# Kernel tuning notes

Hardware: AMD Instinct MI355X
Metric: run time of the kernel (lower is better)

## Reference

```python
import jax, jax.numpy as jnp
import numpy as np

N_PATCH, N_Z, K, BS = 16, 128, 10, 1024
D = N_PATCH * N_Z


def setup_inputs() -> dict:
    key = jax.random.key(0)
    k1, k2, k3, k4 = jax.random.split(key, 4)
    z = jax.random.normal(k1, (BS, D), dtype=jnp.float32)
    m = jax.random.normal(k2, (K, D), dtype=jnp.float32)
    L = jax.random.normal(k3, (K, D, D), dtype=jnp.float32)
    components = jax.random.randint(k4, (BS,), 0, K, dtype=jnp.int64)
    return {"z": z, "m": m, "L": L, "components": components}


def reference(z, m, L, components):
    # samps[k] = m[k] + z @ L[k].T   -> (K, BS, D)
    samps = jnp.einsum('bd,ked->kbe', z, L) + m[:, None, :]
    # one-hot mask-and-sum over components == gather selected expert per sample
    x = samps[components, jnp.arange(z.shape[0])]  # (BS, D)
    return x.reshape(-1, N_PATCH, N_Z)
```

## Files before the change

kernel.cpp:

```cpp
#include <hip/hip_runtime.h>
#include <hip/hip_bf16.h>


#define DDIM  2048
#define BSAMP 1024
#define KCOMP 10
#define MPAD  160

typedef __attribute__((ext_vector_type(8))) short bf16x8;
typedef __attribute__((ext_vector_type(4))) float f32x4;

__device__ __forceinline__ short bfs(float x) {
    __hip_bfloat16 h = __float2bfloat16(x);
    return *reinterpret_cast<short*>(&h);
}

__global__ void build_map(const int* __restrict__ comp,
                          int* __restrict__ rowmap,
                          int* __restrict__ counts) {
    __shared__ int sc[KCOMP];
    const int t = threadIdx.x;
    if (t < KCOMP) sc[t] = 0;
    __syncthreads();
    const int c = comp[t];
    const int r = atomicAdd(&sc[c], 1);
    if (r < MPAD) rowmap[c * MPAD + r] = t;
    __syncthreads();
    if (t < KCOMP) counts[t] = sc[t];
}

__global__ void zprep(const float* __restrict__ z,
                      const int* __restrict__ rowmap,
                      short* __restrict__ zfrag) {
    const int idx  = blockIdx.x * 256 + threadIdx.x;
    const int lane = idx & 63;
    const int rest = idx >> 6;
    const int ms   = rest % 10;
    const int kit  = rest / 10;
    const int it   = kit & 63;
    const int k    = kit >> 6;
    const int slot = ms * 16 + (lane & 15);
    const int r    = rowmap[k * MPAD + slot] & (BSAMP - 1);
    const int d    = it * 32 + (lane >> 4) * 8;
    const float* zp = z + (size_t)r * DDIM + d;
    f32x4 a = *(const f32x4*)zp;
    f32x4 b = *(const f32x4*)(zp + 4);
    bf16x8 o;
#pragma unroll
    for (int j = 0; j < 4; ++j) { o[j] = bfs(a[j]); o[4 + j] = bfs(b[j]); }
    *(bf16x8*)(zfrag + (size_t)idx * 8) = o;
}

template <int MT>
__device__ __forceinline__ void gmm_body(
        const short* __restrict__ Ap,
        const float* __restrict__ Bp,
        const float* __restrict__ mvec,
        const int* __restrict__ rowmap,
        float* __restrict__ out,
        int k, int mh, int e, int cnt, int lane) {
    f32x4 acc[MT];
#pragma unroll
    for (int mt = 0; mt < MT; ++mt) acc[mt] = (f32x4){0.f, 0.f, 0.f, 0.f};

    f32x4 Bw[8][2];
    bf16x8 A0[MT], A1[MT];
#pragma unroll
    for (int j = 0; j < 8; ++j) {
        Bw[j][0] = *(const f32x4*)(Bp + j * 32);
        Bw[j][1] = *(const f32x4*)(Bp + j * 32 + 4);
    }
#pragma unroll
    for (int mt = 0; mt < MT; ++mt) A0[mt] = *(const bf16x8*)(Ap + mt * 512);

    const float* Bpf = Bp + 8 * 32;
    const short* Apf = Ap + 5120;
    int it = 0;

    auto step = [&](bf16x8* Ac, bf16x8* An, f32x4* Bs) {
#pragma unroll
        for (int mt = 0; mt < MT; ++mt) An[mt] = *(const bf16x8*)(Apf + mt * 512);
        f32x4 nb0 = *(const f32x4*)(Bpf);
        f32x4 nb1 = *(const f32x4*)(Bpf + 4);
        bf16x8 b;
#pragma unroll
        for (int j = 0; j < 4; ++j) { b[j] = bfs(Bs[0][j]); b[4 + j] = bfs(Bs[1][j]); }
#pragma unroll
        for (int mt = 0; mt < MT; ++mt)
            acc[mt] = __builtin_amdgcn_mfma_f32_16x16x32_bf16(Ac[mt], b, acc[mt], 0, 0, 0);
        Bs[0] = nb0; Bs[1] = nb1;
        ++it;
        if (it < 63) Apf += 5120;
        if (it < 56) Bpf += 32;
    };

    for (int ot = 0; ot < 8; ++ot) {
        step(A0, A1, Bw[0]); step(A1, A0, Bw[1]);
        step(A0, A1, Bw[2]); step(A1, A0, Bw[3]);
        step(A0, A1, Bw[4]); step(A1, A0, Bw[5]);
        step(A0, A1, Bw[6]); step(A1, A0, Bw[7]);
    }

    const float mu  = mvec[k * DDIM + e];
    const int rquad = (lane >> 4) * 4;
    const int rmB   = k * MPAD;
#pragma unroll
    for (int mt = 0; mt < MT; ++mt) {
        const int sb = mh * 80 + mt * 16 + rquad;
#pragma unroll
        for (int r = 0; r < 4; ++r) {
            const int slot = sb + r;
            if (slot < cnt) {
                const int bidx = rowmap[rmB + slot];
                out[(size_t)bidx * DDIM + e] = acc[mt][r] + mu;
            }
        }
    }
}

__global__ __launch_bounds__(128, 2)
void gmm_direct(const short* __restrict__ zfrag,
                const float* __restrict__ mvec,
                const float* __restrict__ Lmat,
                const int* __restrict__ rowmap,
                const int* __restrict__ counts,
                float* __restrict__ out) {
    const int t = threadIdx.x, lane = t & 63, nh = t >> 6;
    const int n  = blockIdx.x >> 1;
    const int mh = blockIdx.x & 1;
    const int k  = blockIdx.y;
    const int cnt = counts[k];
    const int rem = cnt - mh * 80;
    if (rem <= 0) return;
    const int nmt = (rem >= 80) ? 5 : ((rem + 15) >> 4);

    const int e = n * 32 + nh * 16 + (lane & 15);
    const short* Ap = zfrag + ((size_t)(k * 64) * 10 + mh * 5) * 512 + lane * 8;
    const float* Bp = Lmat + (size_t)k * DDIM * DDIM + (size_t)e * DDIM
                    + (lane >> 4) * 8;

    switch (nmt) {
        case 5: gmm_body<5>(Ap, Bp, mvec, rowmap, out, k, mh, e, cnt, lane); break;
        case 4: gmm_body<4>(Ap, Bp, mvec, rowmap, out, k, mh, e, cnt, lane); break;
        case 3: gmm_body<3>(Ap, Bp, mvec, rowmap, out, k, mh, e, cnt, lane); break;
        case 2: gmm_body<2>(Ap, Bp, mvec, rowmap, out, k, mh, e, cnt, lane); break;
        default: gmm_body<1>(Ap, Bp, mvec, rowmap, out, k, mh, e, cnt, lane); break;
    }
}

__device__ __forceinline__ void async16(void* lds, const void* g) {
    __builtin_amdgcn_global_load_lds(
        (const __attribute__((address_space(1))) void*)g,
        (__attribute__((address_space(3))) void*)lds, 16, 0, 0);
}
__device__ __forceinline__ bf16x8 frag8(const char* base, int o0, int o1) {
    f32x4 x = *(const f32x4*)(base + o0);
    f32x4 y = *(const f32x4*)(base + o1);
    bf16x8 r;
#pragma unroll
    for (int i = 0; i < 4; ++i) { r[i] = bfs(x[i]); r[4 + i] = bfs(y[i]); }
    return r;
}
__global__ __launch_bounds__(256, 2)
void gmm_f32z(const float* __restrict__ z, const float* __restrict__ mvec,
              const float* __restrict__ Lmat, const int* __restrict__ rowmap,
              const int* __restrict__ counts, float* __restrict__ out) {
    __shared__ __attribute__((aligned(16))) char smem[2 * 28672];
    const int t = threadIdx.x, lane = t & 63, w = t >> 6;
    const int mh = w >> 1, nh = w & 1;
    const int k = blockIdx.y, n0 = blockIdx.x * 64;
    const float* Lk = Lmat + (size_t)k * DDIM * DDIM;
    const int rq = t >> 3;
    const int scol = ((t & 7) ^ (rq & 7)) * 4;
    int rm[5];
#pragma unroll
    for (int j = 0; j < 5; ++j)
        rm[j] = rowmap[k * MPAD + j * 32 + rq] & (BSAMP - 1);
    const unsigned ub = (unsigned)(t & ~63) * 16;
    auto stage = [&](int buf, int it) {
        char* lb = smem + buf * 28672;
        const int d0 = it * 32 + scol;
#pragma unroll
        for (int j = 0; j < 5; ++j)
            async16(lb + j * 4096 + ub, z + (size_t)rm[j] * DDIM + d0);
        async16(lb + 20480 + ub,        Lk + (size_t)(n0 + rq) * DDIM + d0);
        async16(lb + 20480 + 4096 + ub, Lk + (size_t)(n0 + 32 + rq) * DDIM + d0);
    };
    f32x4 acc[5][2];
#pragma unroll
    for (int mt = 0; mt < 5; ++mt)
#pragma unroll
        for (int nt = 0; nt < 2; ++nt) acc[mt][nt] = (f32x4){0.f, 0.f, 0.f, 0.f};
    stage(0, 0);
    __syncthreads();
    const int fr = lane & 15, g0 = (lane >> 4) * 2;
    for (int it = 0; it < DDIM / 32; ++it) {
        if (it + 1 < DDIM / 32) stage((it + 1) & 1, it + 1);
        const char* lb = smem + (it & 1) * 28672;
        const int rb0 = nh * 32 + fr, rb1 = rb0 + 16;
        bf16x8 b0 = frag8(lb + 20480, rb0 * 128 + ((g0 ^ rb0) & 7) * 16,
                          rb0 * 128 + (((g0 + 1) ^ rb0) & 7) * 16);
        bf16x8 b1 = frag8(lb + 20480, rb1 * 128 + ((g0 ^ rb1) & 7) * 16,
                          rb1 * 128 + (((g0 + 1) ^ rb1) & 7) * 16);
#pragma unroll
        for (int mt = 0; mt < 5; ++mt) {
            const int ra = mh * 80 + mt * 16 + fr;
            bf16x8 a = frag8(lb, ra * 128 + ((g0 ^ ra) & 7) * 16,
                             ra * 128 + (((g0 + 1) ^ ra) & 7) * 16);
            acc[mt][0] = __builtin_amdgcn_mfma_f32_16x16x32_bf16(a, b0, acc[mt][0], 0, 0, 0);
            acc[mt][1] = __builtin_amdgcn_mfma_f32_16x16x32_bf16(a, b1, acc[mt][1], 0, 0, 0);
        }
        __syncthreads();
    }
    const int cnt = counts[k], rquad = (lane >> 4) * 4;
#pragma unroll
    for (int nt = 0; nt < 2; ++nt) {
        const int e = n0 + nh * 32 + nt * 16 + fr;
        const float mu = mvec[k * DDIM + e];
#pragma unroll
        for (int mt = 0; mt < 5; ++mt) {
            const int sb = mh * 80 + mt * 16 + rquad;
#pragma unroll
            for (int r = 0; r < 4; ++r) {
                const int slot = sb + r;
                if (slot < cnt)
                    out[(size_t)rowmap[k * MPAD + slot] * DDIM + e] = acc[mt][nt][r] + mu;
            }
        }
    }
}

extern "C" void kernel_launch(void* const* d_in, const int* in_sizes, int n_in,
                              void* d_out, int out_size, void* d_ws, size_t ws_size,
                              hipStream_t stream) {
    const float* z    = (const float*)d_in[0];
    const float* mvec = (const float*)d_in[1];
    const float* Lmat = (const float*)d_in[2];
    const int* comp   = (const int*)d_in[3];
    float* out        = (float*)d_out;

    int* rowmap = (int*)d_ws;
    int* counts = rowmap + KCOMP * MPAD;
    build_map<<<1, BSAMP, 0, stream>>>(comp, rowmap, counts);

    const size_t zf_off = 8192;
    const size_t zf_sz  = (size_t)KCOMP * 64 * 10 * 64 * 16;

    if (ws_size >= zf_off + zf_sz) {
        short* zfrag = (short*)((char*)d_ws + zf_off);
        zprep<<<1600, 256, 0, stream>>>(z, rowmap, zfrag);
        gmm_direct<<<dim3(128, KCOMP), 128, 0, stream>>>(
            zfrag, mvec, Lmat, rowmap, counts, out);
    } else {
        gmm_f32z<<<dim3(32, KCOMP), 256, 0, stream>>>(
            z, mvec, Lmat, rowmap, counts, out);
    }
}
```

Baseline: 279.8 us.

## Use single-wave blocks covering all rows per expert with nontemporal L streaming

```diff
diff --git a/kernel.cpp b/kernel.cpp
--- a/kernel.cpp
+++ b/kernel.cpp
@@ -58,47 +58,56 @@
         const float* __restrict__ mvec,
         const int* __restrict__ rowmap,
         float* __restrict__ out,
-        int k, int mh, int e, int cnt, int lane) {
+        int k, int e, int cnt, int lane) {
     f32x4 acc[MT];
 #pragma unroll
     for (int mt = 0; mt < MT; ++mt) acc[mt] = (f32x4){0.f, 0.f, 0.f, 0.f};
 
-    f32x4 Bw[8][2];
+    f32x4 Ba[4][2], Bb[4][2];
     bf16x8 A0[MT], A1[MT];
-#pragma unroll
-    for (int j = 0; j < 8; ++j) {
-        Bw[j][0] = *(const f32x4*)(Bp + j * 32);
-        Bw[j][1] = *(const f32x4*)(Bp + j * 32 + 4);
+
+#pragma unroll
+    for (int j = 0; j < 4; ++j) {
+        Ba[j][0] = __builtin_nontemporal_load((const f32x4*)(Bp + j * 32));
+        Ba[j][1] = __builtin_nontemporal_load((const f32x4*)(Bp + j * 32 + 4));
     }
 #pragma unroll
     for (int mt = 0; mt < MT; ++mt) A0[mt] = *(const bf16x8*)(Ap + mt * 512);
 
-    const float* Bpf = Bp + 8 * 32;
-    const short* Apf = Ap + 5120;
-    int it = 0;
-
-    auto step = [&](bf16x8* Ac, bf16x8* An, f32x4* Bs) {
-#pragma unroll
-        for (int mt = 0; mt < MT; ++mt) An[mt] = *(const bf16x8*)(Apf + mt * 512);
-        f32x4 nb0 = *(const f32x4*)(Bpf);
-        f32x4 nb1 = *(const f32x4*)(Bpf + 4);
-        bf16x8 b;
-#pragma unroll
-        for (int j = 0; j < 4; ++j) { b[j] = bfs(Bs[0][j]); b[4 + j] = bfs(Bs[1][j]); }
-#pragma unroll
-        for (int mt = 0; mt < MT; ++mt)
-            acc[mt] = __builtin_amdgcn_mfma_f32_16x16x32_bf16(Ac[mt], b, acc[mt], 0, 0, 0);
-        Bs[0] = nb0; Bs[1] = nb1;
-        ++it;
-        if (it < 63) Apf += 5120;
-        if (it < 56) Bpf += 32;
+    auto inner4 = [&](f32x4 (*C)[2], f32x4 (*N)[2], int it0) {
+#pragma unroll
+        for (int j = 0; j < 4; ++j) {
+            int tf = it0 + 4 + j; tf = (tf > 63) ? 63 : tf;
+            const float* p = Bp + tf * 32;
+            N[j][0] = __builtin_nontemporal_load((const f32x4*)(p));
+            N[j][1] = __builtin_nontemporal_load((const f32x4*)(p + 4));
+        }
+        __builtin_amdgcn_sched_barrier(0);
+#pragma unroll
+        for (int j = 0; j < 4; ++j) {
+            bf16x8* Ac = (j & 1) ? A1 : A0;
+            bf16x8* An = (j & 1) ? A0 : A1;
+            int ta = it0 + j + 1; ta = (ta > 63) ? 63 : ta;
+            const short* ap = Ap + (size_t)ta * 5120;
+#pragma unroll
+            for (int mt = 0; mt < MT; ++mt)
+                An[mt] = *(const bf16x8*)(ap + mt * 512);
+            bf16x8 b;
+#pragma unroll
+            for (int i = 0; i < 4; ++i) {
+                b[i]     = bfs(C[j][0][i]);
+                b[4 + i] = bfs(C[j][1][i]);
+            }
+#pragma unroll
+            for (int mt = 0; mt < MT; ++mt)
+                acc[mt] = __builtin_amdgcn_mfma_f32_16x16x32_bf16(
+                              Ac[mt], b, acc[mt], 0, 0, 0);
+        }
     };
 
     for (int ot = 0; ot < 8; ++ot) {
-        step(A0, A1, Bw[0]); step(A1, A0, Bw[1]);
-        step(A0, A1, Bw[2]); step(A1, A0, Bw[3]);
-        step(A0, A1, Bw[4]); step(A1, A0, Bw[5]);
-        step(A0, A1, Bw[6]); step(A1, A0, Bw[7]);
+        inner4(Ba, Bb, ot * 8);
+        inner4(Bb, Ba, ot * 8 + 4);
     }
 
     const float mu  = mvec[k * DDIM + e];
@@ -106,10 +115,9 @@
     const int rmB   = k * MPAD;
 #pragma unroll
     for (int mt = 0; mt < MT; ++mt) {
-        const int sb = mh * 80 + mt * 16 + rquad;
 #pragma unroll
         for (int r = 0; r < 4; ++r) {
-            const int slot = sb + r;
+            const int slot = mt * 16 + rquad + r;
             if (slot < cnt) {
                 const int bidx = rowmap[rmB + slot];
                 out[(size_t)bidx * DDIM + e] = acc[mt][r] + mu;
@@ -118,33 +126,43 @@
     }
 }
 
-__global__ __launch_bounds__(128, 2)
+__global__ __launch_bounds__(64, 1)
 void gmm_direct(const short* __restrict__ zfrag,
                 const float* __restrict__ mvec,
                 const float* __restrict__ Lmat,
                 const int* __restrict__ rowmap,
                 const int* __restrict__ counts,
                 float* __restrict__ out) {
-    const int t = threadIdx.x, lane = t & 63, nh = t >> 6;
-    const int n  = blockIdx.x >> 1;
-    const int mh = blockIdx.x & 1;
-    const int k  = blockIdx.y;
+    const int lane = threadIdx.x & 63;
+    const int bid = blockIdx.x;
+    const int x = bid & 7;
+    const int o = bid >> 3;
+    int k, n;
+    if (o < 128) { k = x;               n = o; }
+    else         { const int s = (o - 128) + x * 32;
+                   k = 8 + (s >> 7);    n = s & 127; }
+
     const int cnt = counts[k];
-    const int rem = cnt - mh * 80;
-    if (rem <= 0) return;
-    const int nmt = (rem >= 80) ? 5 : ((rem + 15) >> 4);
-
-    const int e = n * 32 + nh * 16 + (lane & 15);
-    const short* Ap = zfrag + ((size_t)(k * 64) * 10 + mh * 5) * 512 + lane * 8;
+    int mtc = (cnt + 15) >> 4;
+    if (mtc > 10) mtc = 10;
+    if (mtc < 1)  mtc = 1;
+
+    const int e = n * 16 + (lane & 15);
+    const short* Ap = zfrag + (size_t)(k * 64) * 10 * 512 + lane * 8;
     const float* Bp = Lmat + (size_t)k * DDIM * DDIM + (size_t)e * DDIM
                     + (lane >> 4) * 8;
 
-    switch (nmt) {
-        case 5: gmm_body<5>(Ap, Bp, mvec, rowmap, out, k, mh, e, cnt, lane); break;
-        case 4: gmm_body<4>(Ap, Bp, mvec, rowmap, out, k, mh, e, cnt, lane); break;
-        case 3: gmm_body<3>(Ap, Bp, mvec, rowmap, out, k, mh, e, cnt, lane); break;
-        case 2: gmm_body<2>(Ap, Bp, mvec, rowmap, out, k, mh, e, cnt, lane); break;
-        default: gmm_body<1>(Ap, Bp, mvec, rowmap, out, k, mh, e, cnt, lane); break;
+    switch (mtc) {
+        case 10: gmm_body<10>(Ap, Bp, mvec, rowmap, out, k, e, cnt, lane); break;
+        case 9:  gmm_body<9 >(Ap, Bp, mvec, rowmap, out, k, e, cnt, lane); break;
+        case 8:  gmm_body<8 >(Ap, Bp, mvec, rowmap, out, k, e, cnt, lane); break;
+        case 7:  gmm_body<7 >(Ap, Bp, mvec, rowmap, out, k, e, cnt, lane); break;
+        case 6:  gmm_body<6 >(Ap, Bp, mvec, rowmap, out, k, e, cnt, lane); break;
+        case 5:  gmm_body<5 >(Ap, Bp, mvec, rowmap, out, k, e, cnt, lane); break;
+        case 4:  gmm_body<4 >(Ap, Bp, mvec, rowmap, out, k, e, cnt, lane); break;
+        case 3:  gmm_body<3 >(Ap, Bp, mvec, rowmap, out, k, e, cnt, lane); break;
+        case 2:  gmm_body<2 >(Ap, Bp, mvec, rowmap, out, k, e, cnt, lane); break;
+        default: gmm_body<1 >(Ap, Bp, mvec, rowmap, out, k, e, cnt, lane); break;
     }
 }
 
@@ -249,7 +267,7 @@
     if (ws_size >= zf_off + zf_sz) {
         short* zfrag = (short*)((char*)d_ws + zf_off);
         zprep<<<1600, 256, 0, stream>>>(z, rowmap, zfrag);
-        gmm_direct<<<dim3(128, KCOMP), 128, 0, stream>>>(
+        gmm_direct<<<1280, 64, 0, stream>>>(
             zfrag, mvec, Lmat, rowmap, counts, out);
     } else {
         gmm_f32z<<<dim3(32, KCOMP), 256, 0, stream>>>(
```

Measured after the change: 273.9 us. -2.1%, faster.
